# Kernel optimization log

Hardware: AMD Instinct MI355X
Metric: run time of the kernel (lower is better)

The kernel has to match this reference:

```python
import jax, jax.numpy as jnp
import numpy as np

EMBED_DIM = 64  # matches init_kwargs embed_dim; used for 1/sqrt(d) scaling


def setup_inputs() -> dict:
    key = jax.random.key(0)
    k1, k2, k3, k4 = jax.random.split(key, 4)
    N1, N2, C, B = 8192, 8192, EMBED_DIM, 8
    query = jax.random.normal(k1, (N1, C), dtype=jnp.float32)
    key_value = jax.random.normal(k2, (N2, C), dtype=jnp.float32)
    # sorted batch indices so per-batch concat order == input row order
    query_coors = jnp.sort(jax.random.randint(k3, (N1,), 0, B))
    key_value_coors = jnp.sort(jax.random.randint(k4, (N2,), 0, B))
    return {
        "query": query,
        "key_value": key_value,
        "query_coors": query_coors,
        "key_value_coors": key_value_coors,
    }


def reference(query, key_value, query_coors, key_value_coors):
    # Per-batch attention: each query row attends only to key_value rows with
    # the same batch index. Equivalent to the original per-batch loop +
    # chunked softmax(QK^T/sqrt(d)) V, expressed as one masked attention.
    # Dropout is identity (eval mode) for a deterministic correctness baseline.
    scale = 1.0 / jnp.sqrt(jnp.asarray(EMBED_DIM, dtype=query.dtype))
    scores = jnp.einsum("nc,mc->nm", query, key_value) * scale  # [N1, N2]
    same_batch = query_coors[:, None] == key_value_coors[None, :]
    neg_inf = jnp.asarray(-jnp.inf, dtype=scores.dtype)
    scores = jnp.where(same_batch, scores, neg_inf)
    attn = jax.nn.softmax(scores, axis=-1)  # softmax within each batch segment
    out = jnp.einsum("nm,mc->nc", attn, key_value)  # [N1, C]
    return out
```

## Files before the change

### kernel.cpp

```cpp
#include <hip/hip_runtime.h>
#include <hip/hip_bf16.h>

typedef __attribute__((ext_vector_type(8))) short bf16x8;
typedef __attribute__((ext_vector_type(4))) unsigned short u16x4;
typedef __attribute__((ext_vector_type(8))) unsigned short u16x8;
typedef __attribute__((ext_vector_type(4))) float f32x4;
typedef __attribute__((ext_vector_type(2))) float f32x2;

#define NEG_INF (-__builtin_inff())
#define QSCALE (0.125f * 1.4426950408889634f)
#define CONST_M 12.0f
#define NC 8
#define NCL2 3

#define SWZK(a) ((a) ^ ((((((a) >> 7) & 3) | ((((a) >> 10) & 1) << 2)) << 4)))

static __device__ __forceinline__ unsigned short f2bf(float x) {
  union { float f; unsigned u; } v; v.f = x;
  unsigned r = (v.u + 0x7fffu + ((v.u >> 16) & 1u)) >> 16;
  return (unsigned short)r;
}
static __device__ __forceinline__ float bf2f(unsigned short h) {
  union { unsigned u; float f; } v; v.u = ((unsigned)h) << 16;
  return v.f;
}

__global__ __launch_bounds__(256) void prep_kv_kernel(
    const float* __restrict__ kv, const int* __restrict__ kvc,
    unsigned short* __restrict__ kvb, unsigned short* __restrict__ kvt,
    int* __restrict__ seg, int nkv) {
  __shared__ unsigned short tile[16][64];
  const int nb8 = gridDim.x >> 3;
  const int bp = ((gridDim.x & 7) == 0) ? ((blockIdx.x & 7) * nb8 + (blockIdx.x >> 3))
                                        : blockIdx.x;
  const int rowbase = bp * 16;
  const int t = threadIdx.x;
  if (t < 16) {
    int i = rowbase + t;
    if (i < nkv) {
      int c = kvc[i];
      int cp = (i == 0) ? -1 : kvc[i - 1];
      if (c != cp) {
        for (int b = cp + 1; b <= c; ++b) seg[b] = i;
        if (i == 0) for (int b = 0; b < c; ++b) seg[8 + b] = 0;
      }
      int cn = (i == nkv - 1) ? 8 : kvc[i + 1];
      if (c != cn) {
        for (int b = c; b < cn; ++b) seg[8 + b] = i + 1;
        if (i == nkv - 1) for (int b = c + 1; b < 8; ++b) seg[b] = nkv;
      }
    }
  }
  const int r = t >> 4;
  const int c = (t & 15) * 4;
  float4 a = *(const float4*)(kv + (size_t)(rowbase + r) * 64 + c);
  u16x4 v4;
  v4[0] = f2bf(a.x); v4[1] = f2bf(a.y); v4[2] = f2bf(a.z); v4[3] = f2bf(a.w);
  __builtin_nontemporal_store(v4, (u16x4*)(kvb + (size_t)(rowbase + r) * 64 + c));
  *(u16x4*)&tile[r][c] = v4;
  __syncthreads();
  const int d = t & 63;
  const int k0 = (t >> 6) * 4;
  u16x4 wv;
#pragma unroll
  for (int j = 0; j < 4; ++j) wv[j] = tile[k0 + j][d];
  const int blk = rowbase >> 5;
  const int kbase = (rowbase & 31) + k0;
  __builtin_nontemporal_store(wv, (u16x4*)(kvt + (size_t)blk * 2048 + d * 32 + kbase));
}

#define STAGE_LOAD(kvx)                                                        \
  {                                                                            \
    const int kvL_ = (kvx);                                                    \
    const char* src_ = stK ? ((const char*)kvb + (size_t)kvL_ * 128 + soff)    \
                           : ((const char*)kvt + (((size_t)kvL_) >> 5) * 4096 + soff); \
    sreg = *(const f32x4*)src_;                                                \
  }
#define STAGE_WRITE(BUF) { *(f32x4*)(ldsbuf[BUF] + doff) = sreg; }

#define STEP(BUF, kvx)                                                         \
  {                                                                            \
    const int kv0_ = (kvx);                                                    \
    const char* Lb_ = ldsbuf[BUF];                                             \
    bf16x8 kf0_ = *(const bf16x8*)(Lb_ + koff0);                               \
    bf16x8 kf1_ = *(const bf16x8*)(Lb_ + koff1);                               \
    bf16x8 kf2_ = *(const bf16x8*)(Lb_ + koff2);                               \
    bf16x8 kf3_ = *(const bf16x8*)(Lb_ + koff3);                               \
    bf16x8 vf0_ = *(const bf16x8*)(Lb_ + voff0);                               \
    bf16x8 vf1_ = *(const bf16x8*)(Lb_ + voff1);                               \
    bf16x8 vf2_ = *(const bf16x8*)(Lb_ + voff2);                               \
    bf16x8 vf3_ = *(const bf16x8*)(Lb_ + voff3);                               \
    f32x4 z_ = {0, 0, 0, 0};                                                   \
    __builtin_amdgcn_s_setprio(1);                                             \
    f32x4 sT0 = __builtin_amdgcn_mfma_f32_16x16x32_bf16(kf0_, qf0, z_, 0, 0, 0); \
    sT0 = __builtin_amdgcn_mfma_f32_16x16x32_bf16(kf1_, qf1, sT0, 0, 0, 0);    \
    f32x4 sT1 = __builtin_amdgcn_mfma_f32_16x16x32_bf16(kf2_, qf0, z_, 0, 0, 0); \
    sT1 = __builtin_amdgcn_mfma_f32_16x16x32_bf16(kf3_, qf1, sT1, 0, 0, 0);    \
    __builtin_amdgcn_s_setprio(0);                                             \
    float v_[8];                                                               \
    const bool full_ = uniformb && (kv0_ >= kv_lo) && (kv0_ + 32 <= kv_hi);    \
    if (full_) {                                                               \
      _Pragma("unroll") for (int r = 0; r < 4; ++r) {                          \
        v_[r] = sT0[r]; v_[4 + r] = sT1[r];                                    \
      }                                                                        \
    } else {                                                                   \
      const int kb0_ = kv0_ + g8;                                              \
      _Pragma("unroll") for (int r = 0; r < 4; ++r) {                          \
        v_[r]     = (kb0_ + r     >= lo_q && kb0_ + r     < hi_q) ? sT0[r] : NEG_INF; \
        v_[4 + r] = (kb0_ + r + 4 >= lo_q && kb0_ + r + 4 < hi_q) ? sT1[r] : NEG_INF; \
      }                                                                        \
    }                                                                          \
    float t_ = fmaxf(fmaxf(fmaxf(v_[0], v_[1]), fmaxf(v_[2], v_[3])),          \
                     fmaxf(fmaxf(v_[4], v_[5]), fmaxf(v_[6], v_[7])));         \
    if (__builtin_expect(__any(t_ > m), 0)) {                                  \
      float tt_ = fmaxf(t_, __shfl_xor(t_, 16));                               \
      tt_ = fmaxf(tt_, __shfl_xor(tt_, 32));                                   \
      float mn_ = fmaxf(m, tt_);                                               \
      float f_ = __builtin_exp2f(m - mn_);                                     \
      l *= f_;                                                                 \
      _Pragma("unroll") for (int r = 0; r < 4; ++r) {                          \
        acc0[r] *= f_; acc1[r] *= f_; acc2[r] *= f_; acc3[r] *= f_;            \
      }                                                                        \
      m = mn_;                                                                 \
    }                                                                          \
    float e_[8];                                                               \
    _Pragma("unroll") for (int i = 0; i < 8; ++i)                              \
      e_[i] = __builtin_exp2f(v_[i] - m);                                      \
    l += (((e_[0] + e_[1]) + (e_[2] + e_[3])) +                                \
          ((e_[4] + e_[5]) + (e_[6] + e_[7])));                                \
    bf16x8 pa_;                                                                \
    _Pragma("unroll") for (int j = 0; j < 8; ++j) pa_[j] = (short)f2bf(e_[j]); \
    __builtin_amdgcn_s_setprio(1);                                             \
    acc0 = __builtin_amdgcn_mfma_f32_16x16x32_bf16(vf0_, pa_, acc0, 0, 0, 0);  \
    acc1 = __builtin_amdgcn_mfma_f32_16x16x32_bf16(vf1_, pa_, acc1, 0, 0, 0);  \
    acc2 = __builtin_amdgcn_mfma_f32_16x16x32_bf16(vf2_, pa_, acc2, 0, 0, 0);  \
    acc3 = __builtin_amdgcn_mfma_f32_16x16x32_bf16(vf3_, pa_, acc3, 0, 0, 0);  \
    __builtin_amdgcn_s_setprio(0);                                             \
  }

__global__ __launch_bounds__(512, 4) void attn_kernel(
    const float* __restrict__ qf,
    const unsigned short* __restrict__ kvb,
    const unsigned short* __restrict__ kvt,
    const int* __restrict__ qc,
    const int* __restrict__ seg,
    unsigned short* __restrict__ pacc,
    float* __restrict__ pml,
    int n2)
{
  __shared__ __attribute__((aligned(16))) char ldsbuf[2][8192];

  const int per8 = gridDim.x >> 3;
  const int ii = ((gridDim.x & 7) == 0) ? ((blockIdx.x & 7) * per8 + (blockIdx.x >> 3))
                                        : blockIdx.x;
  const int qt = ii >> NCL2;
  const int c  = ii & (NC - 1);
  const int qbase = qt << 7;

  const int tid = threadIdx.x;
  const int w = tid >> 6;
  const int lane = tid & 63;
  const int q16 = lane & 15;
  const int g = lane >> 4;
  const int g8 = g * 8;
  const int q0w = qbase + w * 16;

  const bool stK = tid < 256;
  const int soff = (tid & 255) * 16;
  const int doff = stK ? SWZK(soff) : 4096 + soff;
  f32x4 sreg;

  const int myb = qc[q0w + q16];
  const int lo_q = seg[myb];
  const int hi_q = seg[8 + myb];
  const int bfirst = qc[qbase];
  const int blast  = qc[qbase + 127];
  const int kv_lo  = seg[bfirst];
  const int kv_hi  = seg[8 + blast];
  const bool uniformb = (bfirst == blast);

  bf16x8 qf0, qf1;
  {
    const float* qr = qf + (size_t)(q0w + q16) * 64 + g8;
    float4 a0 = *(const float4*)(qr),      a1 = *(const float4*)(qr + 4);
    float4 a2 = *(const float4*)(qr + 32), a3 = *(const float4*)(qr + 36);
    qf0[0]=(short)f2bf(a0.x*QSCALE); qf0[1]=(short)f2bf(a0.y*QSCALE);
    qf0[2]=(short)f2bf(a0.z*QSCALE); qf0[3]=(short)f2bf(a0.w*QSCALE);
    qf0[4]=(short)f2bf(a1.x*QSCALE); qf0[5]=(short)f2bf(a1.y*QSCALE);
    qf0[6]=(short)f2bf(a1.z*QSCALE); qf0[7]=(short)f2bf(a1.w*QSCALE);
    qf1[0]=(short)f2bf(a2.x*QSCALE); qf1[1]=(short)f2bf(a2.y*QSCALE);
    qf1[2]=(short)f2bf(a2.z*QSCALE); qf1[3]=(short)f2bf(a2.w*QSCALE);
    qf1[4]=(short)f2bf(a3.x*QSCALE); qf1[5]=(short)f2bf(a3.y*QSCALE);
    qf1[6]=(short)f2bf(a3.z*QSCALE); qf1[7]=(short)f2bf(a3.w*QSCALE);
  }

  const int base = kv_lo & ~31;
  const int nblk = (kv_hi - base + 31) >> 5;
  const int b0i = (nblk * c) >> NCL2;
  const int b1i = (nblk * (c + 1)) >> NCL2;

  const int rowoff = ((q16 >> 2) << 3) + (q16 & 3);
  const int koff0 = SWZK(rowoff * 128 + g * 16);
  const int koff1 = SWZK(rowoff * 128 + 64 + g * 16);
  const int koff2 = SWZK((rowoff + 4) * 128 + g * 16);
  const int koff3 = SWZK((rowoff + 4) * 128 + 64 + g * 16);
  const int voff0 = 4096 + (q16 +  0) * 64 + g * 16;
  const int voff1 = 4096 + (q16 + 16) * 64 + g * 16;
  const int voff2 = 4096 + (q16 + 32) * 64 + g * 16;
  const int voff3 = 4096 + (q16 + 48) * 64 + g * 16;

  f32x4 acc0 = {0,0,0,0}, acc1 = {0,0,0,0}, acc2 = {0,0,0,0}, acc3 = {0,0,0,0};
  float m = CONST_M;
  float l = 0.0f;

  if (b0i < b1i) {
    STAGE_LOAD(base + b0i * 32);
    STAGE_WRITE(0);
    __syncthreads();
    int cur = 0;
    for (int b = b0i; b < b1i; ++b) {
      const bool more = (b + 1 < b1i);
      if (more) STAGE_LOAD(base + (b + 1) * 32);
      STEP(cur, base + b * 32);
      if (more) STAGE_WRITE(cur ^ 1);
      __syncthreads();
      cur ^= 1;
    }
  }

  l += __shfl_xor(l, 16);
  l += __shfl_xor(l, 32);

  const int row = q0w + q16;
  unsigned short* pr = pacc + ((size_t)row * NC + c) * 64;
  u16x4 h0, h1, h2, h3;
#pragma unroll
  for (int r = 0; r < 4; ++r) {
    h0[r] = f2bf(acc0[r]); h1[r] = f2bf(acc1[r]);
    h2[r] = f2bf(acc2[r]); h3[r] = f2bf(acc3[r]);
  }
  __builtin_nontemporal_store(h0, (u16x4*)(pr + 0  + g * 4));
  __builtin_nontemporal_store(h1, (u16x4*)(pr + 16 + g * 4));
  __builtin_nontemporal_store(h2, (u16x4*)(pr + 32 + g * 4));
  __builtin_nontemporal_store(h3, (u16x4*)(pr + 48 + g * 4));
  if (g == 0) {
    f32x2 v; v[0] = m; v[1] = l;
    __builtin_nontemporal_store(v, (f32x2*)(pml + ((size_t)row * NC + c) * 2));
  }
}

__global__ __launch_bounds__(256) void merge_kernel(
    const unsigned short* __restrict__ pacc, const float* __restrict__ pml,
    float* __restrict__ out)
{
  const int nb8 = gridDim.x >> 3;
  const int bq = ((gridDim.x & 7) == 0) ? ((blockIdx.x & 7) * nb8 + (blockIdx.x >> 3))
                                        : blockIdx.x;
  const int q0 = bq * 16;
  const int t = threadIdx.x;
  const int i = t >> 4;
  const int c0 = (t & 15) * 4;
  const int R = q0 + i;

  float mm[NC], ll[NC], sc[NC];
  float mstar = NEG_INF;
#pragma unroll
  for (int cc = 0; cc < NC; ++cc) {
    f32x2 v = *(const f32x2*)(pml + ((size_t)R * NC + cc) * 2);
    mm[cc] = v[0]; ll[cc] = v[1];
    mstar = fmaxf(mstar, v[0]);
  }
  float L = 0.0f;
#pragma unroll
  for (int cc = 0; cc < NC; ++cc) {
    sc[cc] = __builtin_exp2f(mm[cc] - mstar);
    L += sc[cc] * ll[cc];
  }
  float inv = (L > 0.0f) ? 1.0f / L : 0.0f;
  f32x4 num = {0, 0, 0, 0};
#pragma unroll
  for (int cc = 0; cc < NC; ++cc) {
    u16x4 a = *(const u16x4*)&pacc[((size_t)R * NC + cc) * 64 + c0];
    float s = sc[cc];
    num[0] += s * bf2f(a[0]); num[1] += s * bf2f(a[1]);
    num[2] += s * bf2f(a[2]); num[3] += s * bf2f(a[3]);
  }
  f32x4 o;
  o[0] = num[0] * inv; o[1] = num[1] * inv;
  o[2] = num[2] * inv; o[3] = num[3] * inv;
  *(f32x4*)&out[(size_t)R * 64 + c0] = o;
}

extern "C" void kernel_launch(void* const* d_in, const int* in_sizes, int n_in,
                              void* d_out, int out_size, void* d_ws, size_t ws_size,
                              hipStream_t stream) {
  const float* q  = (const float*)d_in[0];
  const float* kv = (const float*)d_in[1];
  const int* qc   = (const int*)d_in[2];
  const int* kvc  = (const int*)d_in[3];
  float* out = (float*)d_out;

  const int C = 64;
  const int n1 = in_sizes[0] / C;
  const int n2 = in_sizes[1] / C;

  char* ws = (char*)d_ws;
  size_t off = 0;
  unsigned short* kvb = (unsigned short*)(ws + off); off += (size_t)n2 * C * 2;
  unsigned short* kvt = (unsigned short*)(ws + off); off += (size_t)n2 * C * 2;
  int* seg = (int*)(ws + off); off += 4096;
  unsigned short* pacc = (unsigned short*)(ws + off); off += (size_t)n1 * NC * 64 * 2;
  float* pml = (float*)(ws + off);

  prep_kv_kernel<<<n2 / 16, 256, 0, stream>>>(kv, kvc, kvb, kvt, seg, n2);
  attn_kernel<<<(n1 / 128) * NC, 512, 0, stream>>>(q, kvb, kvt, qc, seg, pacc, pml, n2);
  merge_kernel<<<n1 / 16, 256, 0, stream>>>(pacc, pml, out);
}
```

Baseline: 25.73 us.

## Process two 16-row query tiles per wave to reuse K/V LDS fragments

Each wave now handles 32 query rows as two independent 16-row sub-tiles with separate softmax state and accumulators, so the block covers 256 query rows. Every K/V fragment loaded from LDS feeds twice as many MFMAs, which cuts LDS traffic and staging loads per unit of work and halves the grid. In exchange register pressure roughly doubles for accumulators and Q fragments, which may hurt occupancy under launch_bounds(512,4). The grid also has fewer blocks, 256 instead of 512, which could leave CUs underfilled.

```diff
diff --git a/kernel.cpp b/kernel.cpp
--- a/kernel.cpp
+++ b/kernel.cpp
@@ -78,6 +78,48 @@
   }
 #define STAGE_WRITE(BUF) { *(f32x4*)(ldsbuf[BUF] + doff) = sreg; }
 
+#define PROC(S, sT0_, sT1_)                                                    \
+  {                                                                            \
+    float v_[8];                                                               \
+    if (full_) {                                                               \
+      _Pragma("unroll") for (int r = 0; r < 4; ++r) {                          \
+        v_[r] = sT0_[r]; v_[4 + r] = sT1_[r];                                  \
+      }                                                                        \
+    } else {                                                                   \
+      _Pragma("unroll") for (int r = 0; r < 4; ++r) {                          \
+        v_[r]     = (kb0_ + r     >= lo##S && kb0_ + r     < hi##S) ? sT0_[r] : NEG_INF; \
+        v_[4 + r] = (kb0_ + r + 4 >= lo##S && kb0_ + r + 4 < hi##S) ? sT1_[r] : NEG_INF; \
+      }                                                                        \
+    }                                                                          \
+    float t_ = fmaxf(fmaxf(fmaxf(v_[0], v_[1]), fmaxf(v_[2], v_[3])),          \
+                     fmaxf(fmaxf(v_[4], v_[5]), fmaxf(v_[6], v_[7])));         \
+    if (__builtin_expect(__any(t_ > m##S), 0)) {                               \
+      float tt_ = fmaxf(t_, __shfl_xor(t_, 16));                               \
+      tt_ = fmaxf(tt_, __shfl_xor(tt_, 32));                                   \
+      float mn_ = fmaxf(m##S, tt_);                                            \
+      float f_ = __builtin_exp2f(m##S - mn_);                                  \
+      l##S *= f_;                                                              \
+      _Pragma("unroll") for (int r = 0; r < 4; ++r) {                          \
+        acc##S##0[r] *= f_; acc##S##1[r] *= f_;                                \
+        acc##S##2[r] *= f_; acc##S##3[r] *= f_;                                \
+      }                                                                        \
+      m##S = mn_;                                                              \
+    }                                                                          \
+    float e_[8];                                                               \
+    _Pragma("unroll") for (int i = 0; i < 8; ++i)                              \
+      e_[i] = __builtin_exp2f(v_[i] - m##S);                                   \
+    l##S += (((e_[0] + e_[1]) + (e_[2] + e_[3])) +                             \
+             ((e_[4] + e_[5]) + (e_[6] + e_[7])));                             \
+    bf16x8 pa_;                                                                \
+    _Pragma("unroll") for (int j = 0; j < 8; ++j) pa_[j] = (short)f2bf(e_[j]); \
+    __builtin_amdgcn_s_setprio(1);                                             \
+    acc##S##0 = __builtin_amdgcn_mfma_f32_16x16x32_bf16(vf0_, pa_, acc##S##0, 0, 0, 0); \
+    acc##S##1 = __builtin_amdgcn_mfma_f32_16x16x32_bf16(vf1_, pa_, acc##S##1, 0, 0, 0); \
+    acc##S##2 = __builtin_amdgcn_mfma_f32_16x16x32_bf16(vf2_, pa_, acc##S##2, 0, 0, 0); \
+    acc##S##3 = __builtin_amdgcn_mfma_f32_16x16x32_bf16(vf3_, pa_, acc##S##3, 0, 0, 0); \
+    __builtin_amdgcn_s_setprio(0);                                             \
+  }
+
 #define STEP(BUF, kvx)                                                         \
   {                                                                            \
     const int kv0_ = (kvx);                                                    \
@@ -92,50 +134,19 @@
     bf16x8 vf3_ = *(const bf16x8*)(Lb_ + voff3);                               \
     f32x4 z_ = {0, 0, 0, 0};                                                   \
     __builtin_amdgcn_s_setprio(1);                                             \
-    f32x4 sT0 = __builtin_amdgcn_mfma_f32_16x16x32_bf16(kf0_, qf0, z_, 0, 0, 0); \
-    sT0 = __builtin_amdgcn_mfma_f32_16x16x32_bf16(kf1_, qf1, sT0, 0, 0, 0);    \
-    f32x4 sT1 = __builtin_amdgcn_mfma_f32_16x16x32_bf16(kf2_, qf0, z_, 0, 0, 0); \
-    sT1 = __builtin_amdgcn_mfma_f32_16x16x32_bf16(kf3_, qf1, sT1, 0, 0, 0);    \
+    f32x4 s00 = __builtin_amdgcn_mfma_f32_16x16x32_bf16(kf0_, qf00, z_, 0, 0, 0); \
+    s00 = __builtin_amdgcn_mfma_f32_16x16x32_bf16(kf1_, qf01, s00, 0, 0, 0);   \
+    f32x4 s01 = __builtin_amdgcn_mfma_f32_16x16x32_bf16(kf2_, qf00, z_, 0, 0, 0); \
+    s01 = __builtin_amdgcn_mfma_f32_16x16x32_bf16(kf3_, qf01, s01, 0, 0, 0);   \
+    f32x4 s10 = __builtin_amdgcn_mfma_f32_16x16x32_bf16(kf0_, qf10, z_, 0, 0, 0); \
+    s10 = __builtin_amdgcn_mfma_f32_16x16x32_bf16(kf1_, qf11, s10, 0, 0, 0);   \
+    f32x4 s11 = __builtin_amdgcn_mfma_f32_16x16x32_bf16(kf2_, qf10, z_, 0, 0, 0); \
+    s11 = __builtin_amdgcn_mfma_f32_16x16x32_bf16(kf3_, qf11, s11, 0, 0, 0);   \
     __builtin_amdgcn_s_setprio(0);                                             \
-    float v_[8];                                                               \
     const bool full_ = uniformb && (kv0_ >= kv_lo) && (kv0_ + 32 <= kv_hi);    \
-    if (full_) {                                                               \
-      _Pragma("unroll") for (int r = 0; r < 4; ++r) {                          \
-        v_[r] = sT0[r]; v_[4 + r] = sT1[r];                                    \
-      }                                                                        \
-    } else {                                                                   \
-      const int kb0_ = kv0_ + g8;                                              \
-      _Pragma("unroll") for (int r = 0; r < 4; ++r) {                          \
-        v_[r]     = (kb0_ + r     >= lo_q && kb0_ + r     < hi_q) ? sT0[r] : NEG_INF; \
-        v_[4 + r] = (kb0_ + r + 4 >= lo_q && kb0_ + r + 4 < hi_q) ? sT1[r] : NEG_INF; \
-      }                                                                        \
-    }                                                                          \
-    float t_ = fmaxf(fmaxf(fmaxf(v_[0], v_[1]), fmaxf(v_[2], v_[3])),          \
-                     fmaxf(fmaxf(v_[4], v_[5]), fmaxf(v_[6], v_[7])));         \
-    if (__builtin_expect(__any(t_ > m), 0)) {                                  \
-      float tt_ = fmaxf(t_, __shfl_xor(t_, 16));                               \
-      tt_ = fmaxf(tt_, __shfl_xor(tt_, 32));                                   \
-      float mn_ = fmaxf(m, tt_);                                               \
-      float f_ = __builtin_exp2f(m - mn_);                                     \
-      l *= f_;                                                                 \
-      _Pragma("unroll") for (int r = 0; r < 4; ++r) {                          \
-        acc0[r] *= f_; acc1[r] *= f_; acc2[r] *= f_; acc3[r] *= f_;            \
-      }                                                                        \
-      m = mn_;                                                                 \
-    }                                                                          \
-    float e_[8];                                                               \
-    _Pragma("unroll") for (int i = 0; i < 8; ++i)                              \
-      e_[i] = __builtin_exp2f(v_[i] - m);                                      \
-    l += (((e_[0] + e_[1]) + (e_[2] + e_[3])) +                                \
-          ((e_[4] + e_[5]) + (e_[6] + e_[7])));                                \
-    bf16x8 pa_;                                                                \
-    _Pragma("unroll") for (int j = 0; j < 8; ++j) pa_[j] = (short)f2bf(e_[j]); \
-    __builtin_amdgcn_s_setprio(1);                                             \
-    acc0 = __builtin_amdgcn_mfma_f32_16x16x32_bf16(vf0_, pa_, acc0, 0, 0, 0);  \
-    acc1 = __builtin_amdgcn_mfma_f32_16x16x32_bf16(vf1_, pa_, acc1, 0, 0, 0);  \
-    acc2 = __builtin_amdgcn_mfma_f32_16x16x32_bf16(vf2_, pa_, acc2, 0, 0, 0);  \
-    acc3 = __builtin_amdgcn_mfma_f32_16x16x32_bf16(vf3_, pa_, acc3, 0, 0, 0);  \
-    __builtin_amdgcn_s_setprio(0);                                             \
+    const int kb0_ = kv0_ + g8;                                                \
+    PROC(0, s00, s01)                                                          \
+    PROC(1, s10, s11)                                                          \
   }
 
 __global__ __launch_bounds__(512, 4) void attn_kernel(
@@ -155,7 +166,7 @@
                                         : blockIdx.x;
   const int qt = ii >> NCL2;
   const int c  = ii & (NC - 1);
-  const int qbase = qt << 7;
+  const int qbase = qt << 8;
 
   const int tid = threadIdx.x;
   const int w = tid >> 6;
@@ -163,35 +174,47 @@
   const int q16 = lane & 15;
   const int g = lane >> 4;
   const int g8 = g * 8;
-  const int q0w = qbase + w * 16;
+  const int q0w = qbase + w * 32;
 
   const bool stK = tid < 256;
   const int soff = (tid & 255) * 16;
   const int doff = stK ? SWZK(soff) : 4096 + soff;
   f32x4 sreg;
 
-  const int myb = qc[q0w + q16];
-  const int lo_q = seg[myb];
-  const int hi_q = seg[8 + myb];
+  const int myb0 = qc[q0w + q16];
+  const int myb1 = qc[q0w + 16 + q16];
+  const int lo0 = seg[myb0], hi0 = seg[8 + myb0];
+  const int lo1 = seg[myb1], hi1 = seg[8 + myb1];
   const int bfirst = qc[qbase];
-  const int blast  = qc[qbase + 127];
+  const int blast  = qc[qbase + 255];
   const int kv_lo  = seg[bfirst];
   const int kv_hi  = seg[8 + blast];
   const bool uniformb = (bfirst == blast);
 
-  bf16x8 qf0, qf1;
+  bf16x8 qf00, qf01, qf10, qf11;
   {
-    const float* qr = qf + (size_t)(q0w + q16) * 64 + g8;
-    float4 a0 = *(const float4*)(qr),      a1 = *(const float4*)(qr + 4);
-    float4 a2 = *(const float4*)(qr + 32), a3 = *(const float4*)(qr + 36);
-    qf0[0]=(short)f2bf(a0.x*QSCALE); qf0[1]=(short)f2bf(a0.y*QSCALE);
-    qf0[2]=(short)f2bf(a0.z*QSCALE); qf0[3]=(short)f2bf(a0.w*QSCALE);
-    qf0[4]=(short)f2bf(a1.x*QSCALE); qf0[5]=(short)f2bf(a1.y*QSCALE);
-    qf0[6]=(short)f2bf(a1.z*QSCALE); qf0[7]=(short)f2bf(a1.w*QSCALE);
-    qf1[0]=(short)f2bf(a2.x*QSCALE); qf1[1]=(short)f2bf(a2.y*QSCALE);
-    qf1[2]=(short)f2bf(a2.z*QSCALE); qf1[3]=(short)f2bf(a2.w*QSCALE);
-    qf1[4]=(short)f2bf(a3.x*QSCALE); qf1[5]=(short)f2bf(a3.y*QSCALE);
-    qf1[6]=(short)f2bf(a3.z*QSCALE); qf1[7]=(short)f2bf(a3.w*QSCALE);
+    const float* qr0 = qf + (size_t)(q0w + q16) * 64 + g8;
+    const float* qr1 = qf + (size_t)(q0w + 16 + q16) * 64 + g8;
+    float4 a0 = *(const float4*)(qr0),      a1 = *(const float4*)(qr0 + 4);
+    float4 a2 = *(const float4*)(qr0 + 32), a3 = *(const float4*)(qr0 + 36);
+    float4 b0 = *(const float4*)(qr1),      b1 = *(const float4*)(qr1 + 4);
+    float4 b2 = *(const float4*)(qr1 + 32), b3 = *(const float4*)(qr1 + 36);
+    qf00[0]=(short)f2bf(a0.x*QSCALE); qf00[1]=(short)f2bf(a0.y*QSCALE);
+    qf00[2]=(short)f2bf(a0.z*QSCALE); qf00[3]=(short)f2bf(a0.w*QSCALE);
+    qf00[4]=(short)f2bf(a1.x*QSCALE); qf00[5]=(short)f2bf(a1.y*QSCALE);
+    qf00[6]=(short)f2bf(a1.z*QSCALE); qf00[7]=(short)f2bf(a1.w*QSCALE);
+    qf01[0]=(short)f2bf(a2.x*QSCALE); qf01[1]=(short)f2bf(a2.y*QSCALE);
+    qf01[2]=(short)f2bf(a2.z*QSCALE); qf01[3]=(short)f2bf(a2.w*QSCALE);
+    qf01[4]=(short)f2bf(a3.x*QSCALE); qf01[5]=(short)f2bf(a3.y*QSCALE);
+    qf01[6]=(short)f2bf(a3.z*QSCALE); qf01[7]=(short)f2bf(a3.w*QSCALE);
+    qf10[0]=(short)f2bf(b0.x*QSCALE); qf10[1]=(short)f2bf(b0.y*QSCALE);
+    qf10[2]=(short)f2bf(b0.z*QSCALE); qf10[3]=(short)f2bf(b0.w*QSCALE);
+    qf10[4]=(short)f2bf(b1.x*QSCALE); qf10[5]=(short)f2bf(b1.y*QSCALE);
+    qf10[6]=(short)f2bf(b1.z*QSCALE); qf10[7]=(short)f2bf(b1.w*QSCALE);
+    qf11[0]=(short)f2bf(b2.x*QSCALE); qf11[1]=(short)f2bf(b2.y*QSCALE);
+    qf11[2]=(short)f2bf(b2.z*QSCALE); qf11[3]=(short)f2bf(b2.w*QSCALE);
+    qf11[4]=(short)f2bf(b3.x*QSCALE); qf11[5]=(short)f2bf(b3.y*QSCALE);
+    qf11[6]=(short)f2bf(b3.z*QSCALE); qf11[7]=(short)f2bf(b3.w*QSCALE);
   }
 
   const int base = kv_lo & ~31;
@@ -209,9 +232,10 @@
   const int voff2 = 4096 + (q16 + 32) * 64 + g * 16;
   const int voff3 = 4096 + (q16 + 48) * 64 + g * 16;
 
-  f32x4 acc0 = {0,0,0,0}, acc1 = {0,0,0,0}, acc2 = {0,0,0,0}, acc3 = {0,0,0,0};
-  float m = CONST_M;
-  float l = 0.0f;
+  f32x4 acc00 = {0,0,0,0}, acc01 = {0,0,0,0}, acc02 = {0,0,0,0}, acc03 = {0,0,0,0};
+  f32x4 acc10 = {0,0,0,0}, acc11 = {0,0,0,0}, acc12 = {0,0,0,0}, acc13 = {0,0,0,0};
+  float m0 = CONST_M, l0 = 0.0f;
+  float m1 = CONST_M, l1 = 0.0f;
 
   if (b0i < b1i) {
     STAGE_LOAD(base + b0i * 32);
@@ -228,25 +252,30 @@
     }
   }
 
-  l += __shfl_xor(l, 16);
-  l += __shfl_xor(l, 32);
-
-  const int row = q0w + q16;
-  unsigned short* pr = pacc + ((size_t)row * NC + c) * 64;
-  u16x4 h0, h1, h2, h3;
-#pragma unroll
-  for (int r = 0; r < 4; ++r) {
-    h0[r] = f2bf(acc0[r]); h1[r] = f2bf(acc1[r]);
-    h2[r] = f2bf(acc2[r]); h3[r] = f2bf(acc3[r]);
-  }
-  __builtin_nontemporal_store(h0, (u16x4*)(pr + 0  + g * 4));
-  __builtin_nontemporal_store(h1, (u16x4*)(pr + 16 + g * 4));
-  __builtin_nontemporal_store(h2, (u16x4*)(pr + 32 + g * 4));
-  __builtin_nontemporal_store(h3, (u16x4*)(pr + 48 + g * 4));
-  if (g == 0) {
-    f32x2 v; v[0] = m; v[1] = l;
-    __builtin_nontemporal_store(v, (f32x2*)(pml + ((size_t)row * NC + c) * 2));
-  }
+  l0 += __shfl_xor(l0, 16); l0 += __shfl_xor(l0, 32);
+  l1 += __shfl_xor(l1, 16); l1 += __shfl_xor(l1, 32);
+
+#define WRITEOUT(S, off_)                                                      \
+  {                                                                            \
+    const int row_ = q0w + (off_) + q16;                                       \
+    unsigned short* pr_ = pacc + ((size_t)row_ * NC + c) * 64;                 \
+    u16x4 h0_, h1_, h2_, h3_;                                                  \
+    _Pragma("unroll") for (int r = 0; r < 4; ++r) {                            \
+      h0_[r] = f2bf(acc##S##0[r]); h1_[r] = f2bf(acc##S##1[r]);                \
+      h2_[r] = f2bf(acc##S##2[r]); h3_[r] = f2bf(acc##S##3[r]);                \
+    }                                                                          \
+    __builtin_nontemporal_store(h0_, (u16x4*)(pr_ + 0  + g * 4));              \
+    __builtin_nontemporal_store(h1_, (u16x4*)(pr_ + 16 + g * 4));              \
+    __builtin_nontemporal_store(h2_, (u16x4*)(pr_ + 32 + g * 4));              \
+    __builtin_nontemporal_store(h3_, (u16x4*)(pr_ + 48 + g * 4));              \
+    if (g == 0) {                                                              \
+      f32x2 v_; v_[0] = m##S; v_[1] = l##S;                                    \
+      __builtin_nontemporal_store(v_, (f32x2*)(pml + ((size_t)row_ * NC + c) * 2)); \
+    }                                                                          \
+  }
+  WRITEOUT(0, 0)
+  WRITEOUT(1, 16)
+#undef WRITEOUT
 }
 
 __global__ __launch_bounds__(256) void merge_kernel(
@@ -313,6 +342,6 @@
   float* pml = (float*)(ws + off);
 
   prep_kv_kernel<<<n2 / 16, 256, 0, stream>>>(kv, kvc, kvb, kvt, seg, n2);
-  attn_kernel<<<(n1 / 128) * NC, 512, 0, stream>>>(q, kvb, kvt, qc, seg, pacc, pml, n2);
+  attn_kernel<<<(n1 / 256) * NC, 512, 0, stream>>>(q, kvb, kvt, qc, seg, pacc, pml, n2);
   merge_kernel<<<n1 / 16, 256, 0, stream>>>(pacc, pml, out);
 }
```

After: 30.74 us. 19.5% more time.
